# Performance work log

Hardware: AMD Instinct MI355X
Metric: run time of the kernel (lower is better)

## Reference

```python
import jax, jax.numpy as jnp
import numpy as np

B, H, S_MAX, D = 2, 32, 8192, 128
S_NEW = 512

def setup_inputs() -> dict:
    key = jax.random.key(0)
    k1, k2 = jax.random.split(key)
    return {
        "input_pos": jnp.arange(S_NEW, dtype=jnp.int64 if jax.config.jax_enable_x64 else jnp.int32),
        "k_val": jax.random.normal(k1, (B, H, S_NEW, D), dtype=jnp.float32),
        "v_val": jax.random.normal(k2, (B, H, S_NEW, D), dtype=jnp.float32),
        "k_cache": jnp.zeros((B, H, S_MAX, D), dtype=jnp.float32),
        "kt_cache": jnp.zeros((B, H, D, S_MAX), dtype=jnp.float32),
        "v_cache": jnp.zeros((B, H, S_MAX, D), dtype=jnp.float32),
    }

def reference(input_pos, k_val, v_val, k_cache, kt_cache, v_cache):
    # Scatter-write new K/V (and K^T) into the caches at input_pos.
    k_out = k_cache.at[:, :, input_pos].set(k_val)                      # [B,H,S_max,D]
    kt_out = kt_cache.at[:, :, :, input_pos].set(
        jnp.swapaxes(k_val, -1, -2))                                    # [B,H,D,S_max]
    v_out = v_cache.at[:, :, input_pos].set(v_val)                      # [B,H,S_max,D]
    # Module returns (kt.transpose(-1,-2), k, v)
    return (jnp.swapaxes(kt_out, -1, -2), k_out, v_out)
```

## Files before the change

### kernel.cpp

```cpp
#include <hip/hip_runtime.h>


#define S_MAXC 8192
#define DC     128
#define BHC    64

typedef __attribute__((ext_vector_type(4))) float v4f;

__global__ void init_inv(int* __restrict__ inv) {
    int i = blockIdx.x * blockDim.x + threadIdx.x;
    if (i < S_MAXC) inv[i] = -1;
}

__global__ void scatter_inv(const int* __restrict__ pos, int* __restrict__ inv, int n) {
    int j = blockIdx.x * blockDim.x + threadIdx.x;
    if (j < n) inv[pos[j]] = j;
}

__global__ void __launch_bounds__(256) fused_kv(
        const v4f* __restrict__ k_val,
        const v4f* __restrict__ v_val,
        const v4f* __restrict__ k_cache,
        const v4f* __restrict__ v_cache,
        const float* __restrict__ kt_cache,
        const int*  __restrict__ inv,
        v4f* __restrict__ out0,
        v4f* __restrict__ out1,
        v4f* __restrict__ out2,
        int s_new) {
    __shared__ __align__(16) float tile[32][132];
    const int tid = blockIdx.x;
    const int bh  = tid >> 8;
    const int s0  = (tid & 255) << 5;
    const int t   = threadIdx.x;
    const int q   = t & 7;
    const int r   = t >> 3;

    const float* ktb = kt_cache + (long)bh * DC * S_MAXC;
    #pragma unroll
    for (int p = 0; p < 4; ++p) {
        int d = p * 32 + r;
        v4f vld = __builtin_nontemporal_load(
            (const v4f*)(ktb + (long)d * S_MAXC + s0 + 4 * q));
        tile[4 * q + 0][d] = vld.x;
        tile[4 * q + 1][d] = vld.y;
        tile[4 * q + 2][d] = vld.z;
        tile[4 * q + 3][d] = vld.w;
    }
    __syncthreads();

    const int s = s0 + r;
    const int j = inv[s];
    const long row = (long)bh * S_MAXC + s;
    v4f* o0 = out0 + row * 32;
    v4f* o1 = out1 + row * 32;
    v4f* o2 = out2 + row * 32;
    if (j >= 0) {
        const v4f* kv = k_val + ((long)bh * s_new + j) * 32;
        const v4f* vv = v_val + ((long)bh * s_new + j) * 32;
        #pragma unroll
        for (int m = 0; m < 4; ++m) {
            int c = q + 8 * m;
            v4f kx = kv[c];
            v4f vx = vv[c];
            __builtin_nontemporal_store(kx, o0 + c);
            __builtin_nontemporal_store(kx, o1 + c);
            __builtin_nontemporal_store(vx, o2 + c);
        }
    } else {
        const v4f* kc = k_cache + row * 32;
        const v4f* vc = v_cache + row * 32;
        #pragma unroll
        for (int m = 0; m < 4; ++m) {
            int c = q + 8 * m;
            v4f kx = __builtin_nontemporal_load(kc + c);
            v4f vx = __builtin_nontemporal_load(vc + c);
            v4f tx = *(const v4f*)&tile[r][4 * c];
            __builtin_nontemporal_store(tx, o0 + c);
            __builtin_nontemporal_store(kx, o1 + c);
            __builtin_nontemporal_store(vx, o2 + c);
        }
    }
}

extern "C" void kernel_launch(void* const* d_in, const int* in_sizes, int n_in,
                              void* d_out, int out_size, void* d_ws, size_t ws_size,
                              hipStream_t stream) {
    const int*   input_pos = (const int*)  d_in[0];
    const float* k_val     = (const float*)d_in[1];
    const float* v_val     = (const float*)d_in[2];
    const float* k_cache   = (const float*)d_in[3];
    const float* kt_cache  = (const float*)d_in[4];
    const float* v_cache   = (const float*)d_in[5];
    const int s_new = in_sizes[0];

    const long per_out = (long)BHC * S_MAXC * DC;
    float* out0 = (float*)d_out;
    float* out1 = out0 + per_out;
    float* out2 = out1 + per_out;

    int* inv = (int*)d_ws;

    init_inv<<<S_MAXC / 256, 256, 0, stream>>>(inv);
    scatter_inv<<<(s_new + 255) / 256, 256, 0, stream>>>(input_pos, inv, s_new);

    const int n_tiles = BHC * (S_MAXC / 32);
    fused_kv<<<n_tiles, 256, 0, stream>>>(
        (const v4f*)k_val, (const v4f*)v_val,
        (const v4f*)k_cache, (const v4f*)v_cache,
        kt_cache, inv,
        (v4f*)out0, (v4f*)out1, (v4f*)out2, s_new);
}
```

Measured before the change: 1.255 ms.

## Process eight tiles per block with double-buffered, swizzled transpose staging

Each block now loops over 8 consecutive 32-row tiles instead of one, with LDS double buffering so the next tile's K^T transpose is staged while the current tile is written out. The LDS layout changes from padded rows to an XOR-like rotation swizzle to avoid bank conflicts on the writes and the vector reads. This cuts block count and launch overhead but lowers parallelism and adds a barrier per iteration. It also doubles LDS use per block, which can reduce occupancy on a purely bandwidth-bound copy.

```diff
diff --git a/kernel.cpp b/kernel.cpp
--- a/kernel.cpp
+++ b/kernel.cpp
@@ -4,6 +4,8 @@
 #define S_MAXC 8192
 #define DC     128
 #define BHC    64
+#define TPB    8
+#define NBLK   ((BHC * (S_MAXC / 32)) / TPB)
 
 typedef __attribute__((ext_vector_type(4))) float v4f;
 
@@ -17,6 +19,22 @@
     if (j < n) inv[pos[j]] = j;
 }
 
+__device__ __forceinline__ void stage_tile(
+        const float* __restrict__ ktb, int s0, int q, int r, float* __restrict__ tb) {
+    #pragma unroll
+    for (int p = 0; p < 4; ++p) {
+        int d = p * 32 + r;
+        v4f vld = __builtin_nontemporal_load(
+            (const v4f*)(ktb + (long)d * S_MAXC + s0 + 4 * q));
+        int c = d >> 2, w = d & 3;
+        #pragma unroll
+        for (int u = 0; u < 4; ++u) {
+            int sl = 4 * q + u;
+            tb[sl * 128 + (((c + (sl >> 3)) & 31) << 2) + w] = ((const float*)&vld)[u];
+        }
+    }
+}
+
 __global__ void __launch_bounds__(256) fused_kv(
         const v4f* __restrict__ k_val,
         const v4f* __restrict__ v_val,
@@ -28,58 +46,59 @@
         v4f* __restrict__ out1,
         v4f* __restrict__ out2,
         int s_new) {
-    __shared__ __align__(16) float tile[32][132];
-    const int tid = blockIdx.x;
-    const int bh  = tid >> 8;
-    const int s0  = (tid & 255) << 5;
-    const int t   = threadIdx.x;
-    const int q   = t & 7;
-    const int r   = t >> 3;
+    __shared__ __align__(16) float tile[2][32 * 128];
+    const int t = threadIdx.x;
+    const int q = t & 7;
+    const int r = t >> 3;
+    const int tbase = blockIdx.x * TPB;
+    const int bh = tbase >> 8;
+    const float* ktb = kt_cache + (long)bh * DC * S_MAXC;
 
-    const float* ktb = kt_cache + (long)bh * DC * S_MAXC;
-    #pragma unroll
-    for (int p = 0; p < 4; ++p) {
-        int d = p * 32 + r;
-        v4f vld = __builtin_nontemporal_load(
-            (const v4f*)(ktb + (long)d * S_MAXC + s0 + 4 * q));
-        tile[4 * q + 0][d] = vld.x;
-        tile[4 * q + 1][d] = vld.y;
-        tile[4 * q + 2][d] = vld.z;
-        tile[4 * q + 3][d] = vld.w;
-    }
+    stage_tile(ktb, (tbase & 255) << 5, q, r, &tile[0][0]);
     __syncthreads();
 
-    const int s = s0 + r;
-    const int j = inv[s];
-    const long row = (long)bh * S_MAXC + s;
-    v4f* o0 = out0 + row * 32;
-    v4f* o1 = out1 + row * 32;
-    v4f* o2 = out2 + row * 32;
-    if (j >= 0) {
-        const v4f* kv = k_val + ((long)bh * s_new + j) * 32;
-        const v4f* vv = v_val + ((long)bh * s_new + j) * 32;
-        #pragma unroll
-        for (int m = 0; m < 4; ++m) {
-            int c = q + 8 * m;
-            v4f kx = kv[c];
-            v4f vx = vv[c];
-            __builtin_nontemporal_store(kx, o0 + c);
-            __builtin_nontemporal_store(kx, o1 + c);
-            __builtin_nontemporal_store(vx, o2 + c);
+    for (int it = 0; it < TPB; ++it) {
+        const int s0 = ((tbase + it) & 255) << 5;
+
+        if (it + 1 < TPB)
+            stage_tile(ktb, s0 + 32, q, r, &tile[(it + 1) & 1][0]);
+
+        const float* tb = &tile[it & 1][0];
+        const int sl = r;
+        const int s  = s0 + sl;
+        const int j  = inv[s];
+        const long row = (long)bh * S_MAXC + s;
+        v4f* o0 = out0 + row * 32;
+        v4f* o1 = out1 + row * 32;
+        v4f* o2 = out2 + row * 32;
+        if (j >= 0) {
+            const v4f* kv = k_val + ((long)bh * s_new + j) * 32;
+            const v4f* vv = v_val + ((long)bh * s_new + j) * 32;
+            #pragma unroll
+            for (int m = 0; m < 4; ++m) {
+                int c = q + 8 * m;
+                v4f kx = kv[c];
+                v4f vx = vv[c];
+                __builtin_nontemporal_store(kx, o0 + c);
+                __builtin_nontemporal_store(kx, o1 + c);
+                __builtin_nontemporal_store(vx, o2 + c);
+            }
+        } else {
+            const v4f* kc = k_cache + row * 32;
+            const v4f* vc = v_cache + row * 32;
+            #pragma unroll
+            for (int m = 0; m < 4; ++m) {
+                int c = q + 8 * m;
+                int pc = (c + (sl >> 3)) & 31;
+                v4f kx = __builtin_nontemporal_load(kc + c);
+                v4f vx = __builtin_nontemporal_load(vc + c);
+                v4f tx = *(const v4f*)&tb[sl * 128 + (pc << 2)];
+                __builtin_nontemporal_store(tx, o0 + c);
+                __builtin_nontemporal_store(kx, o1 + c);
+                __builtin_nontemporal_store(vx, o2 + c);
+            }
         }
-    } else {
-        const v4f* kc = k_cache + row * 32;
-        const v4f* vc = v_cache + row * 32;
-        #pragma unroll
-        for (int m = 0; m < 4; ++m) {
-            int c = q + 8 * m;
-            v4f kx = __builtin_nontemporal_load(kc + c);
-            v4f vx = __builtin_nontemporal_load(vc + c);
-            v4f tx = *(const v4f*)&tile[r][4 * c];
-            __builtin_nontemporal_store(tx, o0 + c);
-            __builtin_nontemporal_store(kx, o1 + c);
-            __builtin_nontemporal_store(vx, o2 + c);
-        }
+        __syncthreads();
     }
 }
 
@@ -104,8 +123,7 @@
     init_inv<<<S_MAXC / 256, 256, 0, stream>>>(inv);
     scatter_inv<<<(s_new + 255) / 256, 256, 0, stream>>>(input_pos, inv, s_new);
 
-    const int n_tiles = BHC * (S_MAXC / 32);
-    fused_kv<<<n_tiles, 256, 0, stream>>>(
+    fused_kv<<<NBLK, 256, 0, stream>>>(
         (const v4f*)k_val, (const v4f*)v_val,
         (const v4f*)k_cache, (const v4f*)v_cache,
         kt_cache, inv,
```

Measured after the change: 1.279 ms. No clear change (+1.9%).
